# Performance work log

Measured on AMD Instinct MI355X. Metric: run time of the kernel, lower is better.

The kernel has to match this reference:

```python
import jax, jax.numpy as jnp
import numpy as np

N, NFEAT, NHID, NCLASS, NHEADS = 4096, 512, 64, 128, 8
ALPHA = 0.2
NEG = -9e15


def leaky(x):
    return jnp.where(x > 0, x, ALPHA * x)


def setup_inputs() -> dict:
    key = jax.random.key(0)
    k = jax.random.split(key, 6)
    x = jax.random.normal(k[0], (N, NFEAT), dtype=jnp.float32)
    adj = jax.random.randint(k[1], (N, N), 0, 2, dtype=jnp.int32)
    # per-head params (xavier-ish scale)
    W = jax.random.normal(k[2], (NHEADS, NFEAT, NHID), dtype=jnp.float32) * (1.414 * (2.0 / (NFEAT + NHID)) ** 0.5)
    a = jax.random.normal(k[3], (NHEADS, 2 * NHID), dtype=jnp.float32) * (1.414 * (2.0 / (2 * NHID + 1)) ** 0.5)
    W_out = jax.random.normal(k[4], (NHEADS * NHID, NCLASS), dtype=jnp.float32) * (1.414 * (2.0 / (NHEADS * NHID + NCLASS)) ** 0.5)
    a_out = jax.random.normal(k[5], (2 * NCLASS,), dtype=jnp.float32) * (1.414 * (2.0 / (2 * NCLASS + 1)) ** 0.5)
    return {"x": x, "adj": adj, "W": W, "a": a, "W_out": W_out, "a_out": a_out}


def _gat_layer_multihead(x, adj_mask, W, a):
    # x: [N,F_in], W: [H,F_in,F_out], a: [H,2*F_out]
    h = jnp.einsum('nf,hfo->hno', x, W)           # [H,N,F_out]
    Fo = W.shape[-1]
    a1, a2 = a[:, :Fo], a[:, Fo:]                  # [H,F_out] each
    fi = jnp.einsum('hno,ho->hn', h, a1)           # score contribution of node i
    fj = jnp.einsum('hno,ho->hn', h, a2)
    e = leaky(fi[:, :, None] + fj[:, None, :])     # [H,N,N] == leakyrelu(a . [h_i||h_j])
    e = jnp.where(adj_mask[None], e, NEG)
    att = jax.nn.softmax(e, axis=-1)
    return jnp.einsum('hij,hjo->hio', att, h)      # [H,N,F_out]


def reference(x, adj, W, a, W_out, a_out):
    adj_mask = adj > 0
    # multi-head hidden layer, concat heads (dropout is identity in eval mode)
    hp = _gat_layer_multihead(x, adj_mask, W, a)            # [H,N,NHID]
    xcat = jnp.transpose(hp, (1, 0, 2)).reshape(N, NHEADS * NHID)
    # output attention layer (single head)
    out = _gat_layer_multihead(xcat, adj_mask, W_out[None], a_out[None])[0]  # [N,NCLASS]
    out = jax.nn.elu(out)
    return jax.nn.log_softmax(out, axis=1)
```

## Files before the change

### kernel.cpp

```cpp
#include <hip/hip_runtime.h>
#include <hip/hip_bf16.h>

#define NNODE 4096

typedef __attribute__((ext_vector_type(8))) short bf16x8;
typedef __attribute__((ext_vector_type(4))) float f32x4;
typedef __attribute__((ext_vector_type(4))) unsigned short us4;
typedef __attribute__((ext_vector_type(8))) unsigned short us8;

__device__ __forceinline__ unsigned short f2bf(float x) {
  __hip_bfloat16 b = __float2bfloat16(x);
  return __builtin_bit_cast(unsigned short, b);
}
__device__ __forceinline__ float bf2f(unsigned short u) {
  unsigned int v = ((unsigned int)u) << 16;
  return __builtin_bit_cast(float, v);
}

__global__ __launch_bounds__(256) void packadj(
    const int* __restrict__ adj, unsigned long long* __restrict__ mask) {
  size_t wid = (size_t)blockIdx.x * 4 + (threadIdx.x >> 6);
  int v = adj[wid * 64 + (threadIdx.x & 63)];
  unsigned long long b = __ballot(v != 0);
  if ((threadIdx.x & 63) == 0) mask[wid] = b;
}

__global__ __launch_bounds__(256) void transpose_bf16(
    const float* __restrict__ src, short* __restrict__ dst, int Nr, int Fsrc) {
  __shared__ float tile[64][68];
  const int t  = threadIdx.x;
  const int n0 = blockIdx.x * 64, o0 = blockIdx.y * 64;
  const int h  = blockIdx.z;
  const float* S = src + ((size_t)h * Nr + n0) * Fsrc + o0;
  short* D = dst + ((size_t)h * Fsrc + o0) * Nr + n0;
  const int r = t >> 2, cs = (t & 3) * 16;
  #pragma unroll
  for (int k2 = 0; k2 < 4; ++k2) {
    float4 v = *(const float4*)&S[(size_t)r * Fsrc + cs + k2 * 4];
    *(float4*)&tile[r][cs + k2 * 4] = v;
  }
  __syncthreads();
  const int o = t >> 2, ns = (t & 3) * 16;
  us8 u0, u1;
  #pragma unroll
  for (int e = 0; e < 8; ++e) u0[e] = f2bf(tile[ns + e][o]);
  #pragma unroll
  for (int e = 0; e < 8; ++e) u1[e] = f2bf(tile[ns + 8 + e][o]);
  *(us8*)&D[(size_t)o * Nr + ns]     = u0;
  *(us8*)&D[(size_t)o * Nr + ns + 8] = u1;
}

__global__ __launch_bounds__(256) void gemm_mfma(
    const short* __restrict__ A, const short* __restrict__ Wt,
    short* __restrict__ hTout, int M, int K, int Nfull) {
  __shared__ short As[64][72];
  const int t  = threadIdx.x;
  const int lane = t & 63;
  const int w  = t >> 6;
  const int i0 = blockIdx.x * 64;
  const int c0 = blockIdx.y * 64;
  const int h  = blockIdx.z;
  const short* Bh = Wt + ((size_t)h * Nfull + c0) * K;
  short*       Hh = hTout + (size_t)h * Nfull * M;

  const int R0 = (w >> 1) * 32;
  const int C0 = (w & 1) * 32;
  const int lr = lane & 15;
  const int lk = lane >> 4;

  const int arow = t >> 2;
  const int aseg = (t & 3) * 16;

  f32x4 acc[2][2] = {};

  const short* b00p = &Bh[(size_t)(C0 + lr) * K + lk * 8];
  const short* b10p = &Bh[(size_t)(C0 + 16 + lr) * K + lk * 8];

  bf16x8 bc[4];
  bc[0] = *(const bf16x8*)(b00p);
  bc[1] = *(const bf16x8*)(b10p);
  bc[2] = *(const bf16x8*)(b00p + 32);
  bc[3] = *(const bf16x8*)(b10p + 32);

  for (int k0 = 0; k0 < K; k0 += 64) {
    {
      const short* src = &A[(size_t)(i0 + arow) * K + k0 + aseg];
      us8 u0 = *(const us8*)(src);
      us8 u1 = *(const us8*)(src + 8);
      *(us8*)&As[arow][aseg]     = u0;
      *(us8*)&As[arow][aseg + 8] = u1;
    }
    bf16x8 bn[4];
    {
      int kn = (k0 + 64 < K) ? (k0 + 64) : k0;
      bn[0] = *(const bf16x8*)(b00p + kn);
      bn[1] = *(const bf16x8*)(b10p + kn);
      bn[2] = *(const bf16x8*)(b00p + kn + 32);
      bn[3] = *(const bf16x8*)(b10p + kn + 32);
    }
    __syncthreads();
    #pragma unroll
    for (int kc = 0; kc < 64; kc += 32) {
      bf16x8 a0 = *(const bf16x8*)&As[R0 + lr][kc + lk * 8];
      bf16x8 a1 = *(const bf16x8*)&As[R0 + 16 + lr][kc + lk * 8];
      bf16x8 b0 = bc[(kc >> 5) * 2 + 0];
      bf16x8 b1 = bc[(kc >> 5) * 2 + 1];
      acc[0][0] = __builtin_amdgcn_mfma_f32_16x16x32_bf16(a0, b0, acc[0][0], 0, 0, 0);
      acc[0][1] = __builtin_amdgcn_mfma_f32_16x16x32_bf16(a0, b1, acc[0][1], 0, 0, 0);
      acc[1][0] = __builtin_amdgcn_mfma_f32_16x16x32_bf16(a1, b0, acc[1][0], 0, 0, 0);
      acc[1][1] = __builtin_amdgcn_mfma_f32_16x16x32_bf16(a1, b1, acc[1][1], 0, 0, 0);
    }
    bc[0] = bn[0]; bc[1] = bn[1]; bc[2] = bn[2]; bc[3] = bn[3];
    __syncthreads();
  }

  #pragma unroll
  for (int fa = 0; fa < 2; ++fa) {
    #pragma unroll
    for (int fb = 0; fb < 2; ++fb) {
      int col  = c0 + C0 + fb * 16 + lr;
      int rowb = i0 + R0 + fa * 16 + lk * 4;
      us4 pk;
      #pragma unroll
      for (int reg = 0; reg < 4; ++reg) pk[reg] = f2bf(acc[fa][fb][reg]);
      *(us4*)&Hh[(size_t)col * M + rowb] = pk;
    }
  }
}

template<int F>
__global__ __launch_bounds__(256) void wa_kernel(
    const float* __restrict__ W, const float* __restrict__ a,
    float* __restrict__ wa) {
  const int gid  = blockIdx.x * 4 + (threadIdx.x >> 6);
  const int lane = threadIdx.x & 63;
  const int h = gid >> 9;
  const int k = gid & 511;
  const float* wrow = W + ((size_t)h * 512 + k) * F;
  const float* ah = a + h * 2 * F;
  float v1 = 0.f, v2 = 0.f;
  #pragma unroll
  for (int o = lane; o < F; o += 64) {
    float wv = wrow[o];
    v1 += wv * ah[o];
    v2 += wv * ah[F + o];
  }
  #pragma unroll
  for (int off = 32; off; off >>= 1) {
    v1 += __shfl_xor(v1, off);
    v2 += __shfl_xor(v2, off);
  }
  if (lane == 0) {
    wa[((size_t)h * 2 + 0) * 512 + k] = v1;
    wa[((size_t)h * 2 + 1) * 512 + k] = v2;
  }
}

__global__ __launch_bounds__(256) void fidot8(
    const float* __restrict__ X, const float* __restrict__ wa,
    short* __restrict__ xbf,
    float* __restrict__ eiP, float* __restrict__ eiN,
    float* __restrict__ ejP, float* __restrict__ ejN) {
  __shared__ float sw[8192];
  for (int idx = threadIdx.x; idx < 8192; idx += 256) sw[idx] = wa[idx];
  __syncthreads();
  const int n    = blockIdx.x * 4 + (threadIdx.x >> 6);
  const int lane = threadIdx.x & 63;
  const float* xr = X + (size_t)n * 512;
  float v[16] = {};
  #pragma unroll
  for (int it = 0; it < 8; ++it) {
    int k = lane + it * 64;
    float xv = xr[k];
    xbf[(size_t)n * 512 + k] = f2bf(xv);
    #pragma unroll
    for (int hh = 0; hh < 8; ++hh) {
      v[2 * hh]     += xv * sw[(2 * hh) * 512 + k];
      v[2 * hh + 1] += xv * sw[(2 * hh + 1) * 512 + k];
    }
  }
  #pragma unroll
  for (int off = 32; off; off >>= 1)
    #pragma unroll
    for (int i = 0; i < 16; ++i) v[i] += __shfl_xor(v[i], off);
  if (lane == 0) {
    #pragma unroll
    for (int hh = 0; hh < 8; ++hh) {
      int idx = hh * NNODE + n;
      float f1 = v[2 * hh], f2 = v[2 * hh + 1];
      eiP[idx] = __expf(f1); eiN[idx] = __expf(0.2f * f1);
      ejP[idx] = __expf(f2); ejN[idx] = __expf(0.2f * f2);
    }
  }
}

template<int OT, int JLEN>
__global__ __launch_bounds__(256) void pv_split(
    const short* __restrict__ hT,
    const float* __restrict__ eiP, const float* __restrict__ eiN,
    const float* __restrict__ ejP, const float* __restrict__ ejN,
    const unsigned long long* __restrict__ mask,
    short* __restrict__ pnum, float* __restrict__ pl, int Fh) {
  __shared__ short hTl[OT][64][72];
  __shared__ float ejPL[64], ejNL[64];

  const int t      = threadIdx.x;
  const int lane   = t & 63;
  const int w      = t >> 6;
  const int i0     = blockIdx.x * 64;
  const int chunk  = blockIdx.y;
  const int nchunk = gridDim.y;
  const int h      = blockIdx.z;
  const int hN     = h * NNODE;
  const short* hTs = hT + (size_t)h * Fh * NNODE;

  const int lr = lane & 15;
  const int lk = lane >> 4;
  const int arow = i0 + w * 16 + lr;
  const float eiPr = eiP[hN + arow];
  const float eiNr = eiN[hN + arow];
  const unsigned long long* mrow = mask + (size_t)arow * (NNODE / 64);

  us8 onesu;
  #pragma unroll
  for (int e = 0; e < 8; ++e) onesu[e] = 0x3F80;
  const bf16x8 ones = __builtin_bit_cast(bf16x8, onesu);

  f32x4 acc[OT][4] = {};
  f32x4 accL = {};

  const int jbase = chunk * JLEN;
  for (int jt = 0; jt < JLEN; jt += 64) {
    const int j0 = jbase + jt;
    {
      const int o = t >> 2, seg = t & 3;
      #pragma unroll
      for (int ot = 0; ot < OT; ++ot) {
        const short* src = hTs + (size_t)(ot * 64 + o) * NNODE + j0 + seg * 16;
        float4 v0 = *(const float4*)(src);
        float4 v1 = *(const float4*)(src + 8);
        *(float4*)&hTl[ot][o][seg * 16]     = v0;
        *(float4*)&hTl[ot][o][seg * 16 + 8] = v1;
      }
    }
    if (t < 64) {
      ejPL[t] = ejP[hN + j0 + t];
      ejNL[t] = ejN[hN + j0 + t];
    }
    __syncthreads();

    const unsigned long long mw = mrow[j0 >> 6];
    #pragma unroll
    for (int kk = 0; kk < 2; ++kk) {
      const int kb = kk * 32 + lk * 8;
      float4 eP0 = *(const float4*)&ejPL[kb];
      float4 eP1 = *(const float4*)&ejPL[kb + 4];
      float4 eN0 = *(const float4*)&ejNL[kb];
      float4 eN1 = *(const float4*)&ejNL[kb + 4];
      const unsigned int mb = (unsigned int)(mw >> kb) & 0xFFu;
      float pv[8];
      pv[0] = fmaxf(eiPr * eP0.x, eiNr * eN0.x);
      pv[1] = fmaxf(eiPr * eP0.y, eiNr * eN0.y);
      pv[2] = fmaxf(eiPr * eP0.z, eiNr * eN0.z);
      pv[3] = fmaxf(eiPr * eP0.w, eiNr * eN0.w);
      pv[4] = fmaxf(eiPr * eP1.x, eiNr * eN1.x);
      pv[5] = fmaxf(eiPr * eP1.y, eiNr * eN1.y);
      pv[6] = fmaxf(eiPr * eP1.z, eiNr * eN1.z);
      pv[7] = fmaxf(eiPr * eP1.w, eiNr * eN1.w);
      us8 af;
      #pragma unroll
      for (int e = 0; e < 8; ++e)
        af[e] = f2bf((mb & (1u << e)) ? pv[e] : 0.0f);
      bf16x8 a = __builtin_bit_cast(bf16x8, af);
      accL = __builtin_amdgcn_mfma_f32_16x16x32_bf16(a, ones, accL, 0, 0, 0);
      #pragma unroll
      for (int ot = 0; ot < OT; ++ot) {
        #pragma unroll
        for (int c = 0; c < 4; ++c) {
          bf16x8 b = *(const bf16x8*)&hTl[ot][c * 16 + lr][kb];
          acc[ot][c] = __builtin_amdgcn_mfma_f32_16x16x32_bf16(a, b, acc[ot][c], 0, 0, 0);
        }
      }
    }
    __syncthreads();
  }

  if (lr == 0) {
    #pragma unroll
    for (int reg = 0; reg < 4; ++reg)
      pl[(size_t)(h * nchunk + chunk) * NNODE + i0 + w * 16 + lk * 4 + reg] = accL[reg];
  }

  short* pout = pnum + ((size_t)(h * nchunk + chunk) * NNODE + i0) * (OT * 64);
  #pragma unroll
  for (int ot = 0; ot < OT; ++ot) {
    #pragma unroll
    for (int c = 0; c < 4; ++c) {
      #pragma unroll
      for (int reg = 0; reg < 4; ++reg) {
        int row = w * 16 + lk * 4 + reg;
        int col = ot * 64 + c * 16 + lr;
        pout[(size_t)row * (OT * 64) + col] = f2bf(acc[ot][c][reg]);
      }
    }
  }
}

__global__ __launch_bounds__(256) void combine1_fidot(
    const short* __restrict__ pnum, const float* __restrict__ pl,
    const float* __restrict__ wa2, short* __restrict__ xcatbf,
    float* __restrict__ eiP2, float* __restrict__ eiN2,
    float* __restrict__ ejP2, float* __restrict__ ejN2) {
  const int n = blockIdx.x, t = threadIdx.x;
  float d1 = 0.f, d2 = 0.f;
  #pragma unroll
  for (int rep = 0; rep < 2; ++rep) {
    int col = t + rep * 256;
    int h = col >> 6, o = col & 63;
    float s = 0.f, L = 0.f;
    #pragma unroll
    for (int c = 0; c < 4; ++c) {
      s += bf2f((unsigned short)pnum[((size_t)(h * 4 + c) * NNODE + n) * 64 + o]);
      L += pl[(size_t)(h * 4 + c) * NNODE + n];
    }
    float xv = s / L;
    xcatbf[(size_t)n * 512 + col] = f2bf(xv);
    d1 += xv * wa2[col];
    d2 += xv * wa2[512 + col];
  }
  #pragma unroll
  for (int off = 32; off; off >>= 1) {
    d1 += __shfl_xor(d1, off);
    d2 += __shfl_xor(d2, off);
  }
  __shared__ float red[2][4];
  if ((t & 63) == 0) { red[0][t >> 6] = d1; red[1][t >> 6] = d2; }
  __syncthreads();
  if (t == 0) {
    float f1 = red[0][0] + red[0][1] + red[0][2] + red[0][3];
    float f2 = red[1][0] + red[1][1] + red[1][2] + red[1][3];
    eiP2[n] = __expf(f1); eiN2[n] = __expf(0.2f * f1);
    ejP2[n] = __expf(f2); ejN2[n] = __expf(0.2f * f2);
  }
}

__global__ __launch_bounds__(128) void combine2_final(
    const short* __restrict__ pnum, const float* __restrict__ pl,
    float* __restrict__ dout) {
  const int n = blockIdx.x, t = threadIdx.x;
  float s = 0.f, L = 0.f;
  #pragma unroll
  for (int c = 0; c < 16; ++c) {
    s += bf2f((unsigned short)pnum[((size_t)c * NNODE + n) * 128 + t]);
    L += pl[(size_t)c * NNODE + n];
  }
  float v = s / L;
  float e = v > 0.f ? v : (__expf(v) - 1.0f);
  float mx = e;
  #pragma unroll
  for (int off = 32; off; off >>= 1) mx = fmaxf(mx, __shfl_xor(mx, off));
  __shared__ float r2[2];
  if ((t & 63) == 0) r2[t >> 6] = mx;
  __syncthreads();
  mx = fmaxf(r2[0], r2[1]);
  float sm = __expf(e - mx);
  #pragma unroll
  for (int off = 32; off; off >>= 1) sm += __shfl_xor(sm, off);
  __shared__ float s2[2];
  if ((t & 63) == 0) s2[t >> 6] = sm;
  __syncthreads();
  float sum = s2[0] + s2[1];
  dout[(size_t)n * 128 + t] = e - mx - __logf(sum);
}

extern "C" void kernel_launch(void* const* d_in, const int* in_sizes, int n_in,
                              void* d_out, int out_size, void* d_ws, size_t ws_size,
                              hipStream_t stream) {
  const float* x     = (const float*)d_in[0];
  const int*   adj   = (const int*)d_in[1];
  const float* W     = (const float*)d_in[2];
  const float* a     = (const float*)d_in[3];
  const float* W_out = (const float*)d_in[4];
  const float* a_out = (const float*)d_in[5];
  float* out = (float*)d_out;

  float* ws = (float*)d_ws;
  unsigned long long* mask = (unsigned long long*)ws;
  short* xbf    = (short*)(ws + 524288);
  short* xcatbf = xbf + 2097152;
  short* hT     = xcatbf + 2097152;
  short* pnum   = hT + 2097152;
  float* pl   = (float*)(pnum + 8388608);
  short* Wt1  = (short*)(pl + 131072);
  short* Wt2  = Wt1 + 262144;
  float* wa1  = (float*)(Wt2 + 65536);
  float* wa2  = wa1 + 8192;
  float* eiP1 = wa2 + 1024;
  float* eiN1 = eiP1 + 32768;
  float* ejP1 = eiN1 + 32768;
  float* ejN1 = ejP1 + 32768;
  float* eiP2 = ejN1 + 32768;
  float* eiN2 = eiP2 + 4096;
  float* ejP2 = eiN2 + 4096;
  float* ejN2 = ejP2 + 4096;

  packadj<<<dim3(NNODE * NNODE / 64 / 4), 256, 0, stream>>>(adj, mask);
  transpose_bf16<<<dim3(8, 1, 8), 256, 0, stream>>>(W, Wt1, 512, 64);
  transpose_bf16<<<dim3(8, 2, 1), 256, 0, stream>>>(W_out, Wt2, 512, 128);
  wa_kernel<64><<<dim3(8 * 512 / 4), 256, 0, stream>>>(W, a, wa1);
  wa_kernel<128><<<dim3(512 / 4), 256, 0, stream>>>(W_out, a_out, wa2);

  fidot8<<<dim3(4096 / 4), 256, 0, stream>>>(x, wa1, xbf, eiP1, eiN1, ejP1, ejN1);
  gemm_mfma<<<dim3(64, 1, 8), 256, 0, stream>>>(xbf, Wt1, hT, 4096, 512, 64);
  pv_split<1, 1024><<<dim3(64, 4, 8), 256, 0, stream>>>(hT, eiP1, eiN1, ejP1, ejN1, mask, pnum, pl, 64);
  combine1_fidot<<<dim3(NNODE), 256, 0, stream>>>(pnum, pl, wa2, xcatbf, eiP2, eiN2, ejP2, ejN2);

  gemm_mfma<<<dim3(64, 2, 1), 256, 0, stream>>>(xcatbf, Wt2, hT, 4096, 512, 128);
  pv_split<2, 256><<<dim3(64, 16, 1), 256, 0, stream>>>(hT, eiP2, eiN2, ejP2, ejN2, mask, pnum, pl, 128);
  combine2_final<<<dim3(NNODE), 128, 0, stream>>>(pnum, pl, out);
}
```

Baseline: 239.4 us.

## Halve GEMM row tile and double PV row tile per block

The projection GEMM now uses 32-row tiles, doubling its grid so more blocks run at once. The attention-PV kernel now handles 128 rows per block, two 16-row fragments per wave. Each staged hT tile is reused across twice as many MFMAs, halving its global/LDS loads per output row. The trade-off is more accumulator registers in pv_split (OT=2 doubles to 16 f32x4 accumulators) and a grid half as large, which may lower occupancy.

```diff
diff --git a/kernel.cpp b/kernel.cpp
--- a/kernel.cpp
+++ b/kernel.cpp
@@ -53,25 +53,25 @@
 __global__ __launch_bounds__(256) void gemm_mfma(
     const short* __restrict__ A, const short* __restrict__ Wt,
     short* __restrict__ hTout, int M, int K, int Nfull) {
-  __shared__ short As[64][72];
+  __shared__ short As[32][72];
   const int t  = threadIdx.x;
   const int lane = t & 63;
   const int w  = t >> 6;
-  const int i0 = blockIdx.x * 64;
+  const int i0 = blockIdx.x * 32;
   const int c0 = blockIdx.y * 64;
   const int h  = blockIdx.z;
   const short* Bh = Wt + ((size_t)h * Nfull + c0) * K;
   short*       Hh = hTout + (size_t)h * Nfull * M;
 
-  const int R0 = (w >> 1) * 32;
+  const int R0 = (w >> 1) * 16;
   const int C0 = (w & 1) * 32;
   const int lr = lane & 15;
   const int lk = lane >> 4;
 
-  const int arow = t >> 2;
-  const int aseg = (t & 3) * 16;
-
-  f32x4 acc[2][2] = {};
+  const int arow = t >> 3;
+  const int aseg = (t & 7) * 8;
+
+  f32x4 acc[2] = {};
 
   const short* b00p = &Bh[(size_t)(C0 + lr) * K + lk * 8];
   const short* b10p = &Bh[(size_t)(C0 + 16 + lr) * K + lk * 8];
@@ -85,10 +85,7 @@
   for (int k0 = 0; k0 < K; k0 += 64) {
     {
       const short* src = &A[(size_t)(i0 + arow) * K + k0 + aseg];
-      us8 u0 = *(const us8*)(src);
-      us8 u1 = *(const us8*)(src + 8);
-      *(us8*)&As[arow][aseg]     = u0;
-      *(us8*)&As[arow][aseg + 8] = u1;
+      *(us8*)&As[arow][aseg] = *(const us8*)(src);
     }
     bf16x8 bn[4];
     {
@@ -102,29 +99,23 @@
     #pragma unroll
     for (int kc = 0; kc < 64; kc += 32) {
       bf16x8 a0 = *(const bf16x8*)&As[R0 + lr][kc + lk * 8];
-      bf16x8 a1 = *(const bf16x8*)&As[R0 + 16 + lr][kc + lk * 8];
       bf16x8 b0 = bc[(kc >> 5) * 2 + 0];
       bf16x8 b1 = bc[(kc >> 5) * 2 + 1];
-      acc[0][0] = __builtin_amdgcn_mfma_f32_16x16x32_bf16(a0, b0, acc[0][0], 0, 0, 0);
-      acc[0][1] = __builtin_amdgcn_mfma_f32_16x16x32_bf16(a0, b1, acc[0][1], 0, 0, 0);
-      acc[1][0] = __builtin_amdgcn_mfma_f32_16x16x32_bf16(a1, b0, acc[1][0], 0, 0, 0);
-      acc[1][1] = __builtin_amdgcn_mfma_f32_16x16x32_bf16(a1, b1, acc[1][1], 0, 0, 0);
+      acc[0] = __builtin_amdgcn_mfma_f32_16x16x32_bf16(a0, b0, acc[0], 0, 0, 0);
+      acc[1] = __builtin_amdgcn_mfma_f32_16x16x32_bf16(a0, b1, acc[1], 0, 0, 0);
     }
     bc[0] = bn[0]; bc[1] = bn[1]; bc[2] = bn[2]; bc[3] = bn[3];
     __syncthreads();
   }
 
   #pragma unroll
-  for (int fa = 0; fa < 2; ++fa) {
-    #pragma unroll
-    for (int fb = 0; fb < 2; ++fb) {
-      int col  = c0 + C0 + fb * 16 + lr;
-      int rowb = i0 + R0 + fa * 16 + lk * 4;
-      us4 pk;
-      #pragma unroll
-      for (int reg = 0; reg < 4; ++reg) pk[reg] = f2bf(acc[fa][fb][reg]);
-      *(us4*)&Hh[(size_t)col * M + rowb] = pk;
-    }
+  for (int fb = 0; fb < 2; ++fb) {
+    int col  = c0 + C0 + fb * 16 + lr;
+    int rowb = i0 + R0 + lk * 4;
+    us4 pk;
+    #pragma unroll
+    for (int reg = 0; reg < 4; ++reg) pk[reg] = f2bf(acc[fb][reg]);
+    *(us4*)&Hh[(size_t)col * M + rowb] = pk;
   }
 }
 
@@ -207,7 +198,7 @@
   const int t      = threadIdx.x;
   const int lane   = t & 63;
   const int w      = t >> 6;
-  const int i0     = blockIdx.x * 64;
+  const int i0     = blockIdx.x * 128;
   const int chunk  = blockIdx.y;
   const int nchunk = gridDim.y;
   const int h      = blockIdx.z;
@@ -216,18 +207,20 @@
 
   const int lr = lane & 15;
   const int lk = lane >> 4;
-  const int arow = i0 + w * 16 + lr;
-  const float eiPr = eiP[hN + arow];
-  const float eiNr = eiN[hN + arow];
-  const unsigned long long* mrow = mask + (size_t)arow * (NNODE / 64);
+  const int r0 = i0 + w * 32 + lr;
+  const int r1 = r0 + 16;
+  const float eiPr0 = eiP[hN + r0], eiNr0 = eiN[hN + r0];
+  const float eiPr1 = eiP[hN + r1], eiNr1 = eiN[hN + r1];
+  const unsigned long long* mrow0 = mask + (size_t)r0 * (NNODE / 64);
+  const unsigned long long* mrow1 = mask + (size_t)r1 * (NNODE / 64);
 
   us8 onesu;
   #pragma unroll
   for (int e = 0; e < 8; ++e) onesu[e] = 0x3F80;
   const bf16x8 ones = __builtin_bit_cast(bf16x8, onesu);
 
-  f32x4 acc[OT][4] = {};
-  f32x4 accL = {};
+  f32x4 acc[OT][2][4] = {};
+  f32x4 accL[2] = {};
 
   const int jbase = chunk * JLEN;
   for (int jt = 0; jt < JLEN; jt += 64) {
@@ -249,7 +242,8 @@
     }
     __syncthreads();
 
-    const unsigned long long mw = mrow[j0 >> 6];
+    const unsigned long long mw0 = mrow0[j0 >> 6];
+    const unsigned long long mw1 = mrow1[j0 >> 6];
     #pragma unroll
     for (int kk = 0; kk < 2; ++kk) {
       const int kb = kk * 32 + lk * 8;
@@ -257,28 +251,32 @@
       float4 eP1 = *(const float4*)&ejPL[kb + 4];
       float4 eN0 = *(const float4*)&ejNL[kb];
       float4 eN1 = *(const float4*)&ejNL[kb + 4];
-      const unsigned int mb = (unsigned int)(mw >> kb) & 0xFFu;
-      float pv[8];
-      pv[0] = fmaxf(eiPr * eP0.x, eiNr * eN0.x);
-      pv[1] = fmaxf(eiPr * eP0.y, eiNr * eN0.y);
-      pv[2] = fmaxf(eiPr * eP0.z, eiNr * eN0.z);
-      pv[3] = fmaxf(eiPr * eP0.w, eiNr * eN0.w);
-      pv[4] = fmaxf(eiPr * eP1.x, eiNr * eN1.x);
-      pv[5] = fmaxf(eiPr * eP1.y, eiNr * eN1.y);
-      pv[6] = fmaxf(eiPr * eP1.z, eiNr * eN1.z);
-      pv[7] = fmaxf(eiPr * eP1.w, eiNr * eN1.w);
-      us8 af;
+      const unsigned int mb0 = (unsigned int)(mw0 >> kb) & 0xFFu;
+      const unsigned int mb1 = (unsigned int)(mw1 >> kb) & 0xFFu;
+      float pj[8], qj[8];
+      pj[0] = eP0.x; pj[1] = eP0.y; pj[2] = eP0.z; pj[3] = eP0.w;
+      pj[4] = eP1.x; pj[5] = eP1.y; pj[6] = eP1.z; pj[7] = eP1.w;
+      qj[0] = eN0.x; qj[1] = eN0.y; qj[2] = eN0.z; qj[3] = eN0.w;
+      qj[4] = eN1.x; qj[5] = eN1.y; qj[6] = eN1.z; qj[7] = eN1.w;
+      us8 af0, af1;
       #pragma unroll
-      for (int e = 0; e < 8; ++e)
-        af[e] = f2bf((mb & (1u << e)) ? pv[e] : 0.0f);
-      bf16x8 a = __builtin_bit_cast(bf16x8, af);
-      accL = __builtin_amdgcn_mfma_f32_16x16x32_bf16(a, ones, accL, 0, 0, 0);
+      for (int e = 0; e < 8; ++e) {
+        float p0 = fmaxf(eiPr0 * pj[e], eiNr0 * qj[e]);
+        float p1 = fmaxf(eiPr1 * pj[e], eiNr1 * qj[e]);
+        af0[e] = f2bf((mb0 & (1u << e)) ? p0 : 0.0f);
+        af1[e] = f2bf((mb1 & (1u << e)) ? p1 : 0.0f);
+      }
+      bf16x8 a0 = __builtin_bit_cast(bf16x8, af0);
+      bf16x8 a1 = __builtin_bit_cast(bf16x8, af1);
+      accL[0] = __builtin_amdgcn_mfma_f32_16x16x32_bf16(a0, ones, accL[0], 0, 0, 0);
+      accL[1] = __builtin_amdgcn_mfma_f32_16x16x32_bf16(a1, ones, accL[1], 0, 0, 0);
       #pragma unroll
       for (int ot = 0; ot < OT; ++ot) {
         #pragma unroll
         for (int c = 0; c < 4; ++c) {
           bf16x8 b = *(const bf16x8*)&hTl[ot][c * 16 + lr][kb];
-          acc[ot][c] = __builtin_amdgcn_mfma_f32_16x16x32_bf16(a, b, acc[ot][c], 0, 0, 0);
+          acc[ot][0][c] = __builtin_amdgcn_mfma_f32_16x16x32_bf16(a0, b, acc[ot][0][c], 0, 0, 0);
+          acc[ot][1][c] = __builtin_amdgcn_mfma_f32_16x16x32_bf16(a1, b, acc[ot][1][c], 0, 0, 0);
         }
       }
     }
@@ -287,20 +285,26 @@
 
   if (lr == 0) {
     #pragma unroll
-    for (int reg = 0; reg < 4; ++reg)
-      pl[(size_t)(h * nchunk + chunk) * NNODE + i0 + w * 16 + lk * 4 + reg] = accL[reg];
+    for (int fa = 0; fa < 2; ++fa)
+      #pragma unroll
+      for (int reg = 0; reg < 4; ++reg)
+        pl[(size_t)(h * nchunk + chunk) * NNODE + i0 + w * 32 + fa * 16 + lk * 4 + reg] =
+            accL[fa][reg];
   }
 
   short* pout = pnum + ((size_t)(h * nchunk + chunk) * NNODE + i0) * (OT * 64);
   #pragma unroll
   for (int ot = 0; ot < OT; ++ot) {
     #pragma unroll
-    for (int c = 0; c < 4; ++c) {
+    for (int fa = 0; fa < 2; ++fa) {
       #pragma unroll
-      for (int reg = 0; reg < 4; ++reg) {
-        int row = w * 16 + lk * 4 + reg;
-        int col = ot * 64 + c * 16 + lr;
-        pout[(size_t)row * (OT * 64) + col] = f2bf(acc[ot][c][reg]);
+      for (int c = 0; c < 4; ++c) {
+        #pragma unroll
+        for (int reg = 0; reg < 4; ++reg) {
+          int row = w * 32 + fa * 16 + lk * 4 + reg;
+          int col = ot * 64 + c * 16 + lr;
+          pout[(size_t)row * (OT * 64) + col] = f2bf(acc[ot][fa][c][reg]);
+        }
       }
     }
   }
@@ -411,11 +415,11 @@
   wa_kernel<128><<<dim3(512 / 4), 256, 0, stream>>>(W_out, a_out, wa2);
 
   fidot8<<<dim3(4096 / 4), 256, 0, stream>>>(x, wa1, xbf, eiP1, eiN1, ejP1, ejN1);
-  gemm_mfma<<<dim3(64, 1, 8), 256, 0, stream>>>(xbf, Wt1, hT, 4096, 512, 64);
-  pv_split<1, 1024><<<dim3(64, 4, 8), 256, 0, stream>>>(hT, eiP1, eiN1, ejP1, ejN1, mask, pnum, pl, 64);
+  gemm_mfma<<<dim3(128, 1, 8), 256, 0, stream>>>(xbf, Wt1, hT, 4096, 512, 64);
+  pv_split<1, 1024><<<dim3(32, 4, 8), 256, 0, stream>>>(hT, eiP1, eiN1, ejP1, ejN1, mask, pnum, pl, 64);
   combine1_fidot<<<dim3(NNODE), 256, 0, stream>>>(pnum, pl, wa2, xcatbf, eiP2, eiN2, ejP2, ejN2);
 
-  gemm_mfma<<<dim3(64, 2, 1), 256, 0, stream>>>(xcatbf, Wt2, hT, 4096, 512, 128);
-  pv_split<2, 256><<<dim3(64, 16, 1), 256, 0, stream>>>(hT, eiP2, eiN2, ejP2, ejN2, mask, pnum, pl, 128);
+  gemm_mfma<<<dim3(128, 2, 1), 256, 0, stream>>>(xcatbf, Wt2, hT, 4096, 512, 128);
+  pv_split<2, 256><<<dim3(32, 16, 1), 256, 0, stream>>>(hT, eiP2, eiN2, ejP2, ejN2, mask, pnum, pl, 128);
   combine2_final<<<dim3(NNODE), 128, 0, stream>>>(pnum, pl, out);
 }
```

Result: no change. 243.3 us (+1.7%).
